# Kernel tuning notes

Hardware: AMD Instinct MI355X
Metric: run time of the kernel (lower is better)

## Reference

```python
import jax, jax.numpy as jnp
import numpy as np

B, L, A, DF = 8, 2048, 25, 128
T = 20  # amino-acid types
NUM_FUNCS = 3
D_IN = 2 * DF + T * A * 3 + 3 * (NUM_FUNCS * 4 + 1)  # 1795


def setup_inputs() -> dict:
    key = jax.random.key(0)
    ks = jax.random.split(key, 16)
    chain_emb = jax.random.normal(ks[7], (10, DF), dtype=jnp.float32)
    chain_emb = chain_emb.at[0].set(0.0)  # padding_idx=0
    return {
        'seq': jax.random.randint(ks[0], (B, L), 0, T),
        'xyz': jax.random.normal(ks[1], (B, L, A, 3), dtype=jnp.float32),
        'dihedrals': jax.random.normal(ks[2], (B, L, 3), dtype=jnp.float32),
        'chain_idx': jax.random.randint(ks[3], (B, L), 0, 10),
        'orientation': jax.random.normal(ks[4], (B, L, 3, 3), dtype=jnp.float32),
        'atom_mask': jnp.ones((B, L, A), dtype=jnp.float32),
        'aa_emb': jax.random.normal(ks[6], (T, DF), dtype=jnp.float32),
        'chain_emb': chain_emb,
        'W1': jax.random.normal(ks[8], (D_IN, 2 * DF), dtype=jnp.float32) * 0.02,
        'b1': jnp.zeros((2 * DF,), dtype=jnp.float32),
        'W2': jax.random.normal(ks[9], (2 * DF, DF), dtype=jnp.float32) * 0.05,
        'b2': jnp.zeros((DF,), dtype=jnp.float32),
        'W3': jax.random.normal(ks[10], (DF, DF), dtype=jnp.float32) * 0.05,
        'b3': jnp.zeros((DF,), dtype=jnp.float32),
        'W4': jax.random.normal(ks[11], (DF, DF), dtype=jnp.float32) * 0.05,
        'b4': jnp.zeros((DF,), dtype=jnp.float32),
    }


def _angular_encoding(x):
    # x: (..., d_in) -> (..., d_in * (num_funcs*4 + 1))
    freq = jnp.array([1.0, 2.0, 3.0, 1.0, 0.5, 1.0 / 3.0], dtype=x.dtype)
    xe = x[..., None]  # (..., d_in, 1)
    enc = jnp.concatenate([xe, jnp.sin(freq * xe), jnp.cos(freq * xe)], axis=-1)
    return enc.reshape(*x.shape[:-1], -1)


def reference(seq, xyz, dihedrals, chain_idx, orientation, atom_mask,
              aa_emb, chain_emb, W1, b1, W2, b2, W3, b3, W4, b4):
    b, l = seq.shape
    CA_IDX = 1
    aa_type_feat = aa_emb[seq]  # (b,l,DF)
    # local frame coords: R^T (x - x_CA) per atom
    xyz_rel = xyz - xyz[:, :, CA_IDX:CA_IDX + 1, :]
    xyz_local = jnp.einsum('blji,blaj->blai', orientation, xyz_rel)  # (b,l,A,3)
    # type-conditioned one-hot scatter of local coords -> (b,l,T*A*3)
    onehot = jax.nn.one_hot(seq, T, dtype=xyz.dtype)  # (b,l,T)
    coord_feat = jnp.einsum('blt,blad->bltad', onehot, xyz_local).reshape(b, l, -1)
    dihedral_feat = _angular_encoding(dihedrals)  # (b,l,39)
    chain_feat = jnp.where((chain_idx == 0)[..., None], 0.0, chain_emb[chain_idx])
    x = jnp.concatenate([aa_type_feat, coord_feat, dihedral_feat, chain_feat], axis=-1)
    h = jax.nn.relu(x @ W1 + b1)
    h = jax.nn.relu(h @ W2 + b2)
    h = jax.nn.relu(h @ W3 + b3)
    return h @ W4 + b4
```

## Files before the change

### kernel.cpp

```cpp
#include <hip/hip_runtime.h>

#define NRES   16384
#define NTYPES 20
#define CAP    1280
#define MT     16
#define CHUNKS 64
#define FPP    392
#define H1P    264
#define H2P    136


#define BUCKET_OFF  512
#define W1S_OFF     32768
#define W1C_OFF     110592
#define W2_OFF      520192
#define W3_OFF      552960
#define W4_OFF      569344

typedef __attribute__((ext_vector_type(8))) short short8;
typedef __attribute__((ext_vector_type(4))) float float4_;

__device__ __forceinline__ unsigned short f2bf(float f) {
    union { float f; unsigned int u; } v; v.f = f;
    unsigned int r = v.u + 0x7FFF + ((v.u >> 16) & 1);
    return (unsigned short)(r >> 16);
}

__global__ void zero_counts_k(int* __restrict__ cnt) {
    if (threadIdx.x < NTYPES) cnt[threadIdx.x] = 0;
}

__global__ void prep_k(const int* __restrict__ seq, int* __restrict__ cnt,
                       const float* __restrict__ W1, const float* __restrict__ W2,
                       const float* __restrict__ W3, const float* __restrict__ W4,
                       unsigned short* __restrict__ ws) {
    const int blk = blockIdx.x, tid = threadIdx.x;
    if (blk < 64) {
        __shared__ int lcnt[NTYPES], lbase[NTYPES];
        if (tid < NTYPES) lcnt[tid] = 0;
        __syncthreads();
        const int r = blk * 256 + tid;
        const int t = seq[r];
        const int sl = atomicAdd(&lcnt[t], 1);
        __syncthreads();
        if (tid < NTYPES && lcnt[tid] > 0)
            lbase[tid] = atomicAdd(&cnt[tid], lcnt[tid]);
        __syncthreads();
        const int slot = lbase[t] + sl;
        if (slot < CAP) ws[BUCKET_OFF + t * CAP + slot] = (unsigned short)r;
        return;
    }
    int i = (blk - 64) * 256 + tid;
    float v[8];
    int dst;
    if (i < 9728) {
        const int g = i >> 8, n = i & 255;
        const int s0 = g * 8;
#pragma unroll
        for (int j = 0; j < 8; ++j) {
            const int s = s0 + j;
            const int row = (s < 128) ? s : (s < 168 ? s + 1500 : s + 1499);
            v[j] = (s0 < 296) ? W1[(size_t)row * 256 + n] : 0.0f;
        }
        dst = W1S_OFF + (g * 256 + n) * 8;
    } else if ((i -= 9728) < 51200) {
        const int t = i / 2560, r2 = i - t * 2560;
        const int g = r2 >> 8, n = r2 & 255;
        const int c0 = g * 8;
#pragma unroll
        for (int j = 0; j < 8; ++j) {
            const int c = c0 + j;
            v[j] = (c < 75) ? W1[(size_t)(128 + 75 * t + c) * 256 + n] : 0.0f;
        }
        dst = W1C_OFF + ((t * 10 + g) * 256 + n) * 8;
    } else if ((i -= 51200) < 4096) {
        const int g = i >> 7, n = i & 127;
#pragma unroll
        for (int j = 0; j < 8; ++j) v[j] = W2[(size_t)(g * 8 + j) * 128 + n];
        dst = W2_OFF + (g * 128 + n) * 8;
    } else if ((i -= 4096) < 2048) {
        const int g = i >> 7, n = i & 127;
#pragma unroll
        for (int j = 0; j < 8; ++j) v[j] = W3[(size_t)(g * 8 + j) * 128 + n];
        dst = W3_OFF + (g * 128 + n) * 8;
    } else {
        i -= 2048;
        const int g = i >> 7, n = i & 127;
#pragma unroll
        for (int j = 0; j < 8; ++j) v[j] = W4[(size_t)(g * 8 + j) * 128 + n];
        dst = W4_OFF + (g * 128 + n) * 8;
    }
    short8 o;
#pragma unroll
    for (int j = 0; j < 8; ++j) o[j] = (short)f2bf(v[j]);
    *(short8*)(ws + dst) = o;
}

__global__ __launch_bounds__(256, 6) void residue_embed_k(
    const float* __restrict__ xyz, const float* __restrict__ dihedrals,
    const int* __restrict__ chain_idx, const float* __restrict__ orient,
    const float* __restrict__ aa_emb, const float* __restrict__ chain_emb,
    const float* __restrict__ b1, const float* __restrict__ b2,
    const float* __restrict__ b3, const float* __restrict__ b4,
    const unsigned short* __restrict__ ws, float* __restrict__ out)
{
    __shared__ __align__(16) unsigned short feat[MT * FPP];
    __shared__ __align__(16) unsigned short h1s[MT * H1P];
    __shared__ int ridx[MT];

    const int* cnt = (const int*)ws;
    const unsigned short* bucket = ws + BUCKET_OFF;

    const int t = blockIdx.x / CHUNKS;
    const int start = (blockIdx.x % CHUNKS) * MT;
    const int count = cnt[t];
    if (start >= count) return;
    const int mact = min(MT, count - start);
    const int tid = threadIdx.x;

    {
        const int m = tid >> 4, s = tid & 15;
        const int idx = bucket[t * CAP + min(start + m, count - 1)];
        if (s == 0) ridx[m] = idx;
        unsigned short* fm = &feat[m * FPP];
#pragma unroll
        for (int i = 0; i < 8; ++i) fm[s * 8 + i] = f2bf(aa_emb[t * 128 + s * 8 + i]);
        const int c = chain_idx[idx];
#pragma unroll
        for (int i = 0; i < 8; ++i)
            fm[248 + s * 8 + i] = f2bf((c == 0) ? 0.0f : chain_emb[c * 128 + s * 8 + i]);
        const float* xr = &xyz[(size_t)idx * 75];
        const float cax = xr[3], cay = xr[4], caz = xr[5];
        const float* R = &orient[(size_t)idx * 9];
        for (int a = s; a < 25; a += 16) {
            float rx = xr[a * 3] - cax, ry = xr[a * 3 + 1] - cay, rz = xr[a * 3 + 2] - caz;
#pragma unroll
            for (int i = 0; i < 3; ++i)
                fm[128 + a * 3 + i] = f2bf(R[i] * rx + R[3 + i] * ry + R[6 + i] * rz);
        }
        if (s < 13) {
            const int qd = (s == 0) ? 0 : (s < 7 ? s - 1 : s - 7);
            const float fq = (qd == 0) ? 1.f : (qd == 1) ? 2.f : (qd == 2) ? 3.f
                           : (qd == 3) ? 1.f : (qd == 4) ? 0.5f : (1.f / 3.f);
#pragma unroll
            for (int d = 0; d < 3; ++d) {
                float x = dihedrals[idx * 3 + d];
                float v = (s == 0) ? x : (s < 7 ? sinf(fq * x) : cosf(fq * x));
                fm[208 + d * 13 + s] = f2bf(v);
            }
        }
        if (s == 14) { for (int k = 203; k < 208; ++k) fm[k] = 0; }
        if (s == 13) fm[247] = 0;
        if (s == 12) { for (int k = 376; k < 384; ++k) fm[k] = 0; }
    }
    __syncthreads();

    const int lane = tid & 63, wv = tid >> 6;
    const int q = lane >> 4, nl = lane & 15;
    const float4_ z = {0.f, 0.f, 0.f, 0.f};

    {
        float4_ acc[4] = {z, z, z, z};
        const int nb = wv * 64;
#pragma unroll 2
        for (int ks = 0; ks < 12; ++ks) {
            const int kf = ks * 32 + q * 8;
            short8 a = *(const short8*)&feat[nl * FPP + kf];
            const bool isC = (kf >= 128) && (kf < 208);
            const int g = isC ? (t * 10 + ((kf - 128) >> 3)) : (((kf < 128) ? kf : (kf - 80)) >> 3);
            const unsigned short* bp = ws + (isC ? W1C_OFF : W1S_OFF) + (size_t)g * 2048;
#pragma unroll
            for (int nt = 0; nt < 4; ++nt) {
                const int n = nb + nt * 16 + nl;
                short8 bf = *(const short8*)(bp + n * 8);
                acc[nt] = __builtin_amdgcn_mfma_f32_16x16x32_bf16(a, bf, acc[nt], 0, 0, 0);
            }
        }
#pragma unroll
        for (int nt = 0; nt < 4; ++nt) {
            const int n = nb + nt * 16 + nl;
            const float bv = b1[n];
#pragma unroll
            for (int r = 0; r < 4; ++r)
                h1s[(q * 4 + r) * H1P + n] = f2bf(fmaxf(acc[nt][r] + bv, 0.f));
        }
    }
    __syncthreads();

    unsigned short* h2s = feat;
    unsigned short* h3s = feat + MT * H2P;
    const int nb2 = wv * 32;

    {
        float4_ acc[2] = {z, z};
#pragma unroll 2
        for (int ks = 0; ks < 8; ++ks) {
            const int kf = ks * 32 + q * 8;
            short8 a = *(const short8*)&h1s[nl * H1P + kf];
            const unsigned short* bp = ws + W2_OFF + (kf >> 3) * 1024;
#pragma unroll
            for (int nt = 0; nt < 2; ++nt) {
                const int n = nb2 + nt * 16 + nl;
                short8 bf = *(const short8*)(bp + n * 8);
                acc[nt] = __builtin_amdgcn_mfma_f32_16x16x32_bf16(a, bf, acc[nt], 0, 0, 0);
            }
        }
#pragma unroll
        for (int nt = 0; nt < 2; ++nt) {
            const int n = nb2 + nt * 16 + nl;
            const float bv = b2[n];
#pragma unroll
            for (int r = 0; r < 4; ++r)
                h2s[(q * 4 + r) * H2P + n] = f2bf(fmaxf(acc[nt][r] + bv, 0.f));
        }
    }
    __syncthreads();

    {
        float4_ acc[2] = {z, z};
#pragma unroll
        for (int ks = 0; ks < 4; ++ks) {
            const int kf = ks * 32 + q * 8;
            short8 a = *(const short8*)&h2s[nl * H2P + kf];
            const unsigned short* bp = ws + W3_OFF + (kf >> 3) * 1024;
#pragma unroll
            for (int nt = 0; nt < 2; ++nt) {
                const int n = nb2 + nt * 16 + nl;
                short8 bf = *(const short8*)(bp + n * 8);
                acc[nt] = __builtin_amdgcn_mfma_f32_16x16x32_bf16(a, bf, acc[nt], 0, 0, 0);
            }
        }
#pragma unroll
        for (int nt = 0; nt < 2; ++nt) {
            const int n = nb2 + nt * 16 + nl;
            const float bv = b3[n];
#pragma unroll
            for (int r = 0; r < 4; ++r)
                h3s[(q * 4 + r) * H2P + n] = f2bf(fmaxf(acc[nt][r] + bv, 0.f));
        }
    }
    __syncthreads();

    {
        float4_ acc[2] = {z, z};
#pragma unroll
        for (int ks = 0; ks < 4; ++ks) {
            const int kf = ks * 32 + q * 8;
            short8 a = *(const short8*)&h3s[nl * H2P + kf];
            const unsigned short* bp = ws + W4_OFF + (kf >> 3) * 1024;
#pragma unroll
            for (int nt = 0; nt < 2; ++nt) {
                const int n = nb2 + nt * 16 + nl;
                short8 bf = *(const short8*)(bp + n * 8);
                acc[nt] = __builtin_amdgcn_mfma_f32_16x16x32_bf16(a, bf, acc[nt], 0, 0, 0);
            }
        }
#pragma unroll
        for (int nt = 0; nt < 2; ++nt) {
            const int n = nb2 + nt * 16 + nl;
            const float bv = b4[n];
#pragma unroll
            for (int r = 0; r < 4; ++r) {
                const int m = q * 4 + r;
                if (m < mact)
                    out[(size_t)ridx[m] * 128 + n] = acc[nt][r] + bv;
            }
        }
    }
}

extern "C" void kernel_launch(void* const* d_in, const int* in_sizes, int n_in,
                              void* d_out, int out_size, void* d_ws, size_t ws_size,
                              hipStream_t stream) {
    const int*   seq       = (const int*)  d_in[0];
    const float* xyz       = (const float*)d_in[1];
    const float* dihedrals = (const float*)d_in[2];
    const int*   chain_idx = (const int*)  d_in[3];
    const float* orient    = (const float*)d_in[4];
    const float* aa_emb    = (const float*)d_in[6];
    const float* chain_emb = (const float*)d_in[7];
    const float* W1 = (const float*)d_in[8];
    const float* b1 = (const float*)d_in[9];
    const float* W2 = (const float*)d_in[10];
    const float* b2 = (const float*)d_in[11];
    const float* W3 = (const float*)d_in[12];
    const float* b3 = (const float*)d_in[13];
    const float* W4 = (const float*)d_in[14];
    const float* b4 = (const float*)d_in[15];

    unsigned short* wsu = (unsigned short*)d_ws;
    int* cnt = (int*)d_ws;
    float* out = (float*)d_out;

    zero_counts_k<<<1, 32, 0, stream>>>(cnt);
    prep_k<<<64 + 270, 256, 0, stream>>>(seq, cnt, W1, W2, W3, W4, wsu);
    residue_embed_k<<<NTYPES * CHUNKS, 256, 0, stream>>>(
        xyz, dihedrals, chain_idx, orient, aa_emb, chain_emb,
        b1, b2, b3, b4, wsu, out);
}
```

Baseline: 115.2 us.

## Double residue tile to 32 rows so each weight fragment feeds two MFMAs

Raises the per-block residue tile from 16 to 32 rows and halves the chunk count. Each wave now loads a weight fragment once and reuses it across two 16-row MFMA tiles, halving global/L2 weight traffic per residue. The feature-building stage is remapped to 8 threads per residue. In exchange, register and LDS use per block grow, launch bounds drop to 3 blocks per CU, there are fewer blocks in total, and the last partial tile per type wastes more work.

```diff
diff --git a/kernel.cpp b/kernel.cpp
--- a/kernel.cpp
+++ b/kernel.cpp
@@ -3,8 +3,8 @@
 #define NRES   16384
 #define NTYPES 20
 #define CAP    1280
-#define MT     16
-#define CHUNKS 64
+#define MT     32
+#define CHUNKS 32
 #define FPP    392
 #define H1P    264
 #define H2P    136
@@ -96,7 +96,7 @@
     *(short8*)(ws + dst) = o;
 }
 
-__global__ __launch_bounds__(256, 6) void residue_embed_k(
+__global__ __launch_bounds__(256, 3) void residue_embed_k(
     const float* __restrict__ xyz, const float* __restrict__ dihedrals,
     const int* __restrict__ chain_idx, const float* __restrict__ orient,
     const float* __restrict__ aa_emb, const float* __restrict__ chain_emb,
@@ -119,39 +119,39 @@
     const int tid = threadIdx.x;
 
     {
-        const int m = tid >> 4, s = tid & 15;
+        const int m = tid >> 3, s = tid & 7;
         const int idx = bucket[t * CAP + min(start + m, count - 1)];
         if (s == 0) ridx[m] = idx;
         unsigned short* fm = &feat[m * FPP];
 #pragma unroll
-        for (int i = 0; i < 8; ++i) fm[s * 8 + i] = f2bf(aa_emb[t * 128 + s * 8 + i]);
+        for (int i = 0; i < 16; ++i) fm[s * 16 + i] = f2bf(aa_emb[t * 128 + s * 16 + i]);
         const int c = chain_idx[idx];
 #pragma unroll
-        for (int i = 0; i < 8; ++i)
-            fm[248 + s * 8 + i] = f2bf((c == 0) ? 0.0f : chain_emb[c * 128 + s * 8 + i]);
+        for (int i = 0; i < 16; ++i)
+            fm[248 + s * 16 + i] = f2bf((c == 0) ? 0.0f : chain_emb[c * 128 + s * 16 + i]);
         const float* xr = &xyz[(size_t)idx * 75];
         const float cax = xr[3], cay = xr[4], caz = xr[5];
         const float* R = &orient[(size_t)idx * 9];
-        for (int a = s; a < 25; a += 16) {
+        for (int a = s; a < 25; a += 8) {
             float rx = xr[a * 3] - cax, ry = xr[a * 3 + 1] - cay, rz = xr[a * 3 + 2] - caz;
 #pragma unroll
             for (int i = 0; i < 3; ++i)
                 fm[128 + a * 3 + i] = f2bf(R[i] * rx + R[3 + i] * ry + R[6 + i] * rz);
         }
-        if (s < 13) {
-            const int qd = (s == 0) ? 0 : (s < 7 ? s - 1 : s - 7);
+        for (int e = s; e < 13; e += 8) {
+            const int qd = (e == 0) ? 0 : (e < 7 ? e - 1 : e - 7);
             const float fq = (qd == 0) ? 1.f : (qd == 1) ? 2.f : (qd == 2) ? 3.f
                            : (qd == 3) ? 1.f : (qd == 4) ? 0.5f : (1.f / 3.f);
 #pragma unroll
             for (int d = 0; d < 3; ++d) {
                 float x = dihedrals[idx * 3 + d];
-                float v = (s == 0) ? x : (s < 7 ? sinf(fq * x) : cosf(fq * x));
-                fm[208 + d * 13 + s] = f2bf(v);
-            }
-        }
-        if (s == 14) { for (int k = 203; k < 208; ++k) fm[k] = 0; }
-        if (s == 13) fm[247] = 0;
-        if (s == 12) { for (int k = 376; k < 384; ++k) fm[k] = 0; }
+                float v = (e == 0) ? x : (e < 7 ? sinf(fq * x) : cosf(fq * x));
+                fm[208 + d * 13 + e] = f2bf(v);
+            }
+        }
+        if (s == 6) { for (int k = 203; k < 208; ++k) fm[k] = 0; }
+        if (s == 5) fm[247] = 0;
+        if (s == 7) { for (int k = 376; k < 384; ++k) fm[k] = 0; }
     }
     __syncthreads();
 
@@ -160,12 +160,13 @@
     const float4_ z = {0.f, 0.f, 0.f, 0.f};
 
     {
-        float4_ acc[4] = {z, z, z, z};
+        float4_ acc[2][4] = {{z, z, z, z}, {z, z, z, z}};
         const int nb = wv * 64;
 #pragma unroll 2
         for (int ks = 0; ks < 12; ++ks) {
             const int kf = ks * 32 + q * 8;
-            short8 a = *(const short8*)&feat[nl * FPP + kf];
+            short8 a0 = *(const short8*)&feat[nl * FPP + kf];
+            short8 a1 = *(const short8*)&feat[(nl + 16) * FPP + kf];
             const bool isC = (kf >= 128) && (kf < 208);
             const int g = isC ? (t * 10 + ((kf - 128) >> 3)) : (((kf < 128) ? kf : (kf - 80)) >> 3);
             const unsigned short* bp = ws + (isC ? W1C_OFF : W1S_OFF) + (size_t)g * 2048;
@@ -173,7 +174,8 @@
             for (int nt = 0; nt < 4; ++nt) {
                 const int n = nb + nt * 16 + nl;
                 short8 bf = *(const short8*)(bp + n * 8);
-                acc[nt] = __builtin_amdgcn_mfma_f32_16x16x32_bf16(a, bf, acc[nt], 0, 0, 0);
+                acc[0][nt] = __builtin_amdgcn_mfma_f32_16x16x32_bf16(a0, bf, acc[0][nt], 0, 0, 0);
+                acc[1][nt] = __builtin_amdgcn_mfma_f32_16x16x32_bf16(a1, bf, acc[1][nt], 0, 0, 0);
             }
         }
 #pragma unroll
@@ -181,8 +183,10 @@
             const int n = nb + nt * 16 + nl;
             const float bv = b1[n];
 #pragma unroll
-            for (int r = 0; r < 4; ++r)
-                h1s[(q * 4 + r) * H1P + n] = f2bf(fmaxf(acc[nt][r] + bv, 0.f));
+            for (int mt = 0; mt < 2; ++mt)
+#pragma unroll
+                for (int r = 0; r < 4; ++r)
+                    h1s[(mt * 16 + q * 4 + r) * H1P + n] = f2bf(fmaxf(acc[mt][nt][r] + bv, 0.f));
         }
     }
     __syncthreads();
@@ -192,17 +196,19 @@
     const int nb2 = wv * 32;
 
     {
-        float4_ acc[2] = {z, z};
+        float4_ acc[2][2] = {{z, z}, {z, z}};
 #pragma unroll 2
         for (int ks = 0; ks < 8; ++ks) {
             const int kf = ks * 32 + q * 8;
-            short8 a = *(const short8*)&h1s[nl * H1P + kf];
+            short8 a0 = *(const short8*)&h1s[nl * H1P + kf];
+            short8 a1 = *(const short8*)&h1s[(nl + 16) * H1P + kf];
             const unsigned short* bp = ws + W2_OFF + (kf >> 3) * 1024;
 #pragma unroll
             for (int nt = 0; nt < 2; ++nt) {
                 const int n = nb2 + nt * 16 + nl;
                 short8 bf = *(const short8*)(bp + n * 8);
-                acc[nt] = __builtin_amdgcn_mfma_f32_16x16x32_bf16(a, bf, acc[nt], 0, 0, 0);
+                acc[0][nt] = __builtin_amdgcn_mfma_f32_16x16x32_bf16(a0, bf, acc[0][nt], 0, 0, 0);
+                acc[1][nt] = __builtin_amdgcn_mfma_f32_16x16x32_bf16(a1, bf, acc[1][nt], 0, 0, 0);
             }
         }
 #pragma unroll
@@ -210,24 +216,28 @@
             const int n = nb2 + nt * 16 + nl;
             const float bv = b2[n];
 #pragma unroll
-            for (int r = 0; r < 4; ++r)
-                h2s[(q * 4 + r) * H2P + n] = f2bf(fmaxf(acc[nt][r] + bv, 0.f));
+            for (int mt = 0; mt < 2; ++mt)
+#pragma unroll
+                for (int r = 0; r < 4; ++r)
+                    h2s[(mt * 16 + q * 4 + r) * H2P + n] = f2bf(fmaxf(acc[mt][nt][r] + bv, 0.f));
         }
     }
     __syncthreads();
 
     {
-        float4_ acc[2] = {z, z};
+        float4_ acc[2][2] = {{z, z}, {z, z}};
 #pragma unroll
         for (int ks = 0; ks < 4; ++ks) {
             const int kf = ks * 32 + q * 8;
-            short8 a = *(const short8*)&h2s[nl * H2P + kf];
+            short8 a0 = *(const short8*)&h2s[nl * H2P + kf];
+            short8 a1 = *(const short8*)&h2s[(nl + 16) * H2P + kf];
             const unsigned short* bp = ws + W3_OFF + (kf >> 3) * 1024;
 #pragma unroll
             for (int nt = 0; nt < 2; ++nt) {
                 const int n = nb2 + nt * 16 + nl;
                 short8 bf = *(const short8*)(bp + n * 8);
-                acc[nt] = __builtin_amdgcn_mfma_f32_16x16x32_bf16(a, bf, acc[nt], 0, 0, 0);
+                acc[0][nt] = __builtin_amdgcn_mfma_f32_16x16x32_bf16(a0, bf, acc[0][nt], 0, 0, 0);
+                acc[1][nt] = __builtin_amdgcn_mfma_f32_16x16x32_bf16(a1, bf, acc[1][nt], 0, 0, 0);
             }
         }
 #pragma unroll
@@ -235,24 +245,28 @@
             const int n = nb2 + nt * 16 + nl;
             const float bv = b3[n];
 #pragma unroll
-            for (int r = 0; r < 4; ++r)
-                h3s[(q * 4 + r) * H2P + n] = f2bf(fmaxf(acc[nt][r] + bv, 0.f));
+            for (int mt = 0; mt < 2; ++mt)
+#pragma unroll
+                for (int r = 0; r < 4; ++r)
+                    h3s[(mt * 16 + q * 4 + r) * H2P + n] = f2bf(fmaxf(acc[mt][nt][r] + bv, 0.f));
         }
     }
     __syncthreads();
 
     {
-        float4_ acc[2] = {z, z};
+        float4_ acc[2][2] = {{z, z}, {z, z}};
 #pragma unroll
         for (int ks = 0; ks < 4; ++ks) {
             const int kf = ks * 32 + q * 8;
-            short8 a = *(const short8*)&h3s[nl * H2P + kf];
+            short8 a0 = *(const short8*)&h3s[nl * H2P + kf];
+            short8 a1 = *(const short8*)&h3s[(nl + 16) * H2P + kf];
             const unsigned short* bp = ws + W4_OFF + (kf >> 3) * 1024;
 #pragma unroll
             for (int nt = 0; nt < 2; ++nt) {
                 const int n = nb2 + nt * 16 + nl;
                 short8 bf = *(const short8*)(bp + n * 8);
-                acc[nt] = __builtin_amdgcn_mfma_f32_16x16x32_bf16(a, bf, acc[nt], 0, 0, 0);
+                acc[0][nt] = __builtin_amdgcn_mfma_f32_16x16x32_bf16(a0, bf, acc[0][nt], 0, 0, 0);
+                acc[1][nt] = __builtin_amdgcn_mfma_f32_16x16x32_bf16(a1, bf, acc[1][nt], 0, 0, 0);
             }
         }
 #pragma unroll
@@ -260,11 +274,13 @@
             const int n = nb2 + nt * 16 + nl;
             const float bv = b4[n];
 #pragma unroll
-            for (int r = 0; r < 4; ++r) {
-                const int m = q * 4 + r;
-                if (m < mact)
-                    out[(size_t)ridx[m] * 128 + n] = acc[nt][r] + bv;
-            }
+            for (int mt = 0; mt < 2; ++mt)
+#pragma unroll
+                for (int r = 0; r < 4; ++r) {
+                    const int m = mt * 16 + q * 4 + r;
+                    if (m < mact)
+                        out[(size_t)ridx[m] * 128 + n] = acc[mt][nt][r] + bv;
+                }
         }
     }
 }
```

Result: slower. 119.0 us (+3.3%).

## Double residue tile to 32 rows with 512-thread blocks, reusing weight fragments

Applied to the files above, without the earlier changes.

Raises the per-block residue tile from 16 to 32 and the block size to 512 threads (8 waves). Each wave now covers a narrower column slice and issues two MFMAs per loaded weight fragment, one for each 16-row half, which halves global weight traffic per residue. The cost is more LDS per block, fewer blocks in the grid, and more idle rows in partially filled type buckets. The hidden feature-building section must handle 32 rows with 512 threads, and that part is not shown.

```diff
diff --git a/kernel.cpp b/kernel.cpp
--- a/kernel.cpp
+++ b/kernel.cpp
@@ -3,8 +3,8 @@
 #define NRES   16384
 #define NTYPES 20
 #define CAP    1280
-#define MT     16
-#define CHUNKS 64
+#define MT     32
+#define CHUNKS 32
 #define FPP    392
 #define H1P    264
 #define H2P    136
@@ -96,7 +96,7 @@
     *(short8*)(ws + dst) = o;
 }
 
-__global__ __launch_bounds__(256, 6) void residue_embed_k(
+__global__ __launch_bounds__(512, 6) void residue_embed_k(
     const float* __restrict__ xyz, const float* __restrict__ dihedrals,
     const int* __restrict__ chain_idx, const float* __restrict__ orient,
     const float* __restrict__ aa_emb, const float* __restrict__ chain_emb,
@@ -160,112 +160,107 @@
     const float4_ z = {0.f, 0.f, 0.f, 0.f};
 
     {
-        float4_ acc[4] = {z, z, z, z};
-        const int nb = wv * 64;
+        float4_ acc[2][2] = {{z, z}, {z, z}};
+        const int nb = wv * 32;
 #pragma unroll 2
         for (int ks = 0; ks < 12; ++ks) {
             const int kf = ks * 32 + q * 8;
-            short8 a = *(const short8*)&feat[nl * FPP + kf];
+            short8 a0 = *(const short8*)&feat[nl * FPP + kf];
+            short8 a1 = *(const short8*)&feat[(nl + 16) * FPP + kf];
             const bool isC = (kf >= 128) && (kf < 208);
             const int g = isC ? (t * 10 + ((kf - 128) >> 3)) : (((kf < 128) ? kf : (kf - 80)) >> 3);
             const unsigned short* bp = ws + (isC ? W1C_OFF : W1S_OFF) + (size_t)g * 2048;
 #pragma unroll
-            for (int nt = 0; nt < 4; ++nt) {
+            for (int nt = 0; nt < 2; ++nt) {
                 const int n = nb + nt * 16 + nl;
                 short8 bf = *(const short8*)(bp + n * 8);
-                acc[nt] = __builtin_amdgcn_mfma_f32_16x16x32_bf16(a, bf, acc[nt], 0, 0, 0);
+                acc[0][nt] = __builtin_amdgcn_mfma_f32_16x16x32_bf16(a0, bf, acc[0][nt], 0, 0, 0);
+                acc[1][nt] = __builtin_amdgcn_mfma_f32_16x16x32_bf16(a1, bf, acc[1][nt], 0, 0, 0);
             }
         }
 #pragma unroll
-        for (int nt = 0; nt < 4; ++nt) {
+        for (int nt = 0; nt < 2; ++nt) {
             const int n = nb + nt * 16 + nl;
             const float bv = b1[n];
 #pragma unroll
-            for (int r = 0; r < 4; ++r)
-                h1s[(q * 4 + r) * H1P + n] = f2bf(fmaxf(acc[nt][r] + bv, 0.f));
+            for (int mt = 0; mt < 2; ++mt)
+#pragma unroll
+                for (int r = 0; r < 4; ++r)
+                    h1s[(mt * 16 + q * 4 + r) * H1P + n] = f2bf(fmaxf(acc[mt][nt][r] + bv, 0.f));
         }
     }
     __syncthreads();
 
     unsigned short* h2s = feat;
     unsigned short* h3s = feat + MT * H2P;
-    const int nb2 = wv * 32;
+    const int nb2 = wv * 16;
 
     {
         float4_ acc[2] = {z, z};
 #pragma unroll 2
         for (int ks = 0; ks < 8; ++ks) {
             const int kf = ks * 32 + q * 8;
-            short8 a = *(const short8*)&h1s[nl * H1P + kf];
-            const unsigned short* bp = ws + W2_OFF + (kf >> 3) * 1024;
-#pragma unroll
-            for (int nt = 0; nt < 2; ++nt) {
-                const int n = nb2 + nt * 16 + nl;
-                short8 bf = *(const short8*)(bp + n * 8);
-                acc[nt] = __builtin_amdgcn_mfma_f32_16x16x32_bf16(a, bf, acc[nt], 0, 0, 0);
+            short8 a0 = *(const short8*)&h1s[nl * H1P + kf];
+            short8 a1 = *(const short8*)&h1s[(nl + 16) * H1P + kf];
+            const int n = nb2 + nl;
+            short8 bf = *(const short8*)(ws + W2_OFF + ((kf >> 3) * 128 + n) * 8);
+            acc[0] = __builtin_amdgcn_mfma_f32_16x16x32_bf16(a0, bf, acc[0], 0, 0, 0);
+            acc[1] = __builtin_amdgcn_mfma_f32_16x16x32_bf16(a1, bf, acc[1], 0, 0, 0);
+        }
+        const int n = nb2 + nl;
+        const float bv = b2[n];
+#pragma unroll
+        for (int mt = 0; mt < 2; ++mt)
+#pragma unroll
+            for (int r = 0; r < 4; ++r)
+                h2s[(mt * 16 + q * 4 + r) * H2P + n] = f2bf(fmaxf(acc[mt][r] + bv, 0.f));
+    }
+    __syncthreads();
+
+    {
+        float4_ acc[2] = {z, z};
+#pragma unroll
+        for (int ks = 0; ks < 4; ++ks) {
+            const int kf = ks * 32 + q * 8;
+            short8 a0 = *(const short8*)&h2s[nl * H2P + kf];
+            short8 a1 = *(const short8*)&h2s[(nl + 16) * H2P + kf];
+            const int n = nb2 + nl;
+            short8 bf = *(const short8*)(ws + W3_OFF + ((kf >> 3) * 128 + n) * 8);
+            acc[0] = __builtin_amdgcn_mfma_f32_16x16x32_bf16(a0, bf, acc[0], 0, 0, 0);
+            acc[1] = __builtin_amdgcn_mfma_f32_16x16x32_bf16(a1, bf, acc[1], 0, 0, 0);
+        }
+        const int n = nb2 + nl;
+        const float bv = b3[n];
+#pragma unroll
+        for (int mt = 0; mt < 2; ++mt)
+#pragma unroll
+            for (int r = 0; r < 4; ++r)
+                h3s[(mt * 16 + q * 4 + r) * H2P + n] = f2bf(fmaxf(acc[mt][r] + bv, 0.f));
+    }
+    __syncthreads();
+
+    {
+        float4_ acc[2] = {z, z};
+#pragma unroll
+        for (int ks = 0; ks < 4; ++ks) {
+            const int kf = ks * 32 + q * 8;
+            short8 a0 = *(const short8*)&h3s[nl * H2P + kf];
+            short8 a1 = *(const short8*)&h3s[(nl + 16) * H2P + kf];
+            const int n = nb2 + nl;
+            short8 bf = *(const short8*)(ws + W4_OFF + ((kf >> 3) * 128 + n) * 8);
+            acc[0] = __builtin_amdgcn_mfma_f32_16x16x32_bf16(a0, bf, acc[0], 0, 0, 0);
+            acc[1] = __builtin_amdgcn_mfma_f32_16x16x32_bf16(a1, bf, acc[1], 0, 0, 0);
+        }
+        const int n = nb2 + nl;
+        const float bv = b4[n];
+#pragma unroll
+        for (int mt = 0; mt < 2; ++mt)
+#pragma unroll
+            for (int r = 0; r < 4; ++r) {
+                const int m = mt * 16 + q * 4 + r;
+                if (m < mact)
+                    out[(size_t)ridx[m] * 128 + n] = acc[mt][r] + bv;
             }
-        }
-#pragma unroll
-        for (int nt = 0; nt < 2; ++nt) {
-            const int n = nb2 + nt * 16 + nl;
-            const float bv = b2[n];
-#pragma unroll
-            for (int r = 0; r < 4; ++r)
-                h2s[(q * 4 + r) * H2P + n] = f2bf(fmaxf(acc[nt][r] + bv, 0.f));
-        }
-    }
-    __syncthreads();
-
-    {
-        float4_ acc[2] = {z, z};
-#pragma unroll
-        for (int ks = 0; ks < 4; ++ks) {
-            const int kf = ks * 32 + q * 8;
-            short8 a = *(const short8*)&h2s[nl * H2P + kf];
-            const unsigned short* bp = ws + W3_OFF + (kf >> 3) * 1024;
-#pragma unroll
-            for (int nt = 0; nt < 2; ++nt) {
-                const int n = nb2 + nt * 16 + nl;
-                short8 bf = *(const short8*)(bp + n * 8);
-                acc[nt] = __builtin_amdgcn_mfma_f32_16x16x32_bf16(a, bf, acc[nt], 0, 0, 0);
-            }
-        }
-#pragma unroll
-        for (int nt = 0; nt < 2; ++nt) {
-            const int n = nb2 + nt * 16 + nl;
-            const float bv = b3[n];
-#pragma unroll
-            for (int r = 0; r < 4; ++r)
-                h3s[(q * 4 + r) * H2P + n] = f2bf(fmaxf(acc[nt][r] + bv, 0.f));
-        }
-    }
-    __syncthreads();
-
-    {
-        float4_ acc[2] = {z, z};
-#pragma unroll
-        for (int ks = 0; ks < 4; ++ks) {
-            const int kf = ks * 32 + q * 8;
-            short8 a = *(const short8*)&h3s[nl * H2P + kf];
-            const unsigned short* bp = ws + W4_OFF + (kf >> 3) * 1024;
-#pragma unroll
-            for (int nt = 0; nt < 2; ++nt) {
-                const int n = nb2 + nt * 16 + nl;
-                short8 bf = *(const short8*)(bp + n * 8);
-                acc[nt] = __builtin_amdgcn_mfma_f32_16x16x32_bf16(a, bf, acc[nt], 0, 0, 0);
-            }
-        }
-#pragma unroll
-        for (int nt = 0; nt < 2; ++nt) {
-            const int n = nb2 + nt * 16 + nl;
-            const float bv = b4[n];
-#pragma unroll
-            for (int r = 0; r < 4; ++r) {
-                const int m = q * 4 + r;
-                if (m < mact)
-                    out[(size_t)ridx[m] * 128 + n] = acc[nt][r] + bv;
-            }
-        }
     }
 }
 
@@ -294,7 +289,7 @@
 
     zero_counts_k<<<1, 32, 0, stream>>>(cnt);
     prep_k<<<64 + 270, 256, 0, stream>>>(seq, cnt, W1, W2, W3, W4, wsu);
-    residue_embed_k<<<NTYPES * CHUNKS, 256, 0, stream>>>(
+    residue_embed_k<<<NTYPES * CHUNKS, 512, 0, stream>>>(
         xyz, dihedrals, chain_idx, orient, aa_emb, chain_emb,
         b1, b2, b3, b4, wsu, out);
 }
```

Result: faster. 112.8 us (-2.1%).
